# Optimization experiments

Hardware: AMD Instinct MI355X
Metric: run time of the kernel (lower is better)

The kernel has to match this reference:

```python
import jax, jax.numpy as jnp
import numpy as np

N = 16384      # nodes
IN_DIM = 256   # input feature dim
H = 256        # hidden dim
K = 16         # kNN neighbors
L = 2          # GCN layers
C = 10         # classes


def setup_inputs() -> dict:
    key = jax.random.key(0)
    ks = jax.random.split(key, 9)
    s = 0.05
    return {
        "x": jax.random.normal(ks[0], (1, N, IN_DIM), jnp.float32),
        "W_pre": jax.random.normal(ks[1], (H, IN_DIM), jnp.float32) * s,
        "b_pre": jnp.zeros((H,), jnp.float32),
        "W_conv": jax.random.normal(ks[2], (L, H, H), jnp.float32) * s,
        "b_conv": jnp.zeros((L, H), jnp.float32),
        "W_fc1": jax.random.normal(ks[3], (H // 2, H), jnp.float32) * s,
        "b_fc1": jnp.zeros((H // 2,), jnp.float32),
        "W_fc2": jax.random.normal(ks[4], (C, H // 2), jnp.float32) * s,
        "b_fc2": jnp.zeros((C,), jnp.float32),
    }


def _knn_edges(h):
    # h: [N, H]. torch.cdist + topk(k+1, largest=False); squared dist preserves order.
    sq = jnp.sum(h * h, axis=-1)                      # [N]
    d2 = sq[:, None] + sq[None, :] - 2.0 * (h @ h.T)  # [N, N]
    _, idx = jax.lax.top_k(-d2, K + 1)                # smallest k+1
    idx = idx[:, 1:]                                  # drop self, [N, K]
    src = jnp.repeat(jnp.arange(N), K)
    dst = idx.reshape(-1)
    # bidirectional edges (cat with flipped), as in build_knn_graph
    s_idx = jnp.concatenate([src, dst])
    t_idx = jnp.concatenate([dst, src])
    return s_idx, t_idx


def _gcn_layer(h, W, b, s_idx, t_idx, norm):
    m = h @ W.T                                             # PyG GCNConv: lin then propagate
    out = jax.ops.segment_sum(m[s_idx] * norm[:, None], t_idx, num_segments=N)
    return out + b


def reference(x, W_pre, b_pre, W_conv, b_conv, W_fc1, b_fc1, W_fc2, b_fc2):
    # pre_fc (dropout inactive in eval)
    h = jax.nn.relu(x @ W_pre.T + b_pre)   # [1, N, H]
    h0 = h[0]                              # B=1
    s_idx, t_idx = _knn_edges(h0)
    # add self loops (GCNConv default)
    loop = jnp.arange(N)
    s_idx = jnp.concatenate([s_idx, loop])
    t_idx = jnp.concatenate([t_idx, loop])
    # symmetric normalization D^{-1/2} (A+I) D^{-1/2}
    deg = jax.ops.segment_sum(jnp.ones_like(s_idx, dtype=h0.dtype), t_idx, num_segments=N)
    dinv = jnp.where(deg > 0, jax.lax.rsqrt(deg), 0.0)
    norm = dinv[s_idx] * dinv[t_idx]
    hf = h0
    for l in range(L):
        hf = jax.nn.relu(_gcn_layer(hf, W_conv[l], b_conv[l], s_idx, t_idx, norm))
    hf = hf[None]                          # [1, N, H]
    hid = jax.nn.relu(hf @ W_fc1.T + b_fc1)
    pred = hid @ W_fc2.T + b_fc2           # [1, N, C]
    return pred
```

## Files before the change

### kernel.cpp

```cpp
#include <hip/hip_runtime.h>

#define NN   16384
#define DIM  256
#define KNN  16
#define SEG  8
#define JT_PER (NN / SEG / 128)

typedef __attribute__((ext_vector_type(8))) short  bf16x8;
typedef __attribute__((ext_vector_type(4))) float  f32x4;

__device__ __forceinline__ void gload_lds16b(const unsigned short* g, void* l)
{
    __builtin_amdgcn_global_load_lds(
        (const __attribute__((address_space(1))) unsigned int*)g,
        (__attribute__((address_space(3))) unsigned int*)l, 16, 0, 0);
}

__device__ __forceinline__ unsigned short f2bf(float x)
{
    unsigned int u = __float_as_uint(x);
    unsigned int r = (u + 0x7fffu + ((u >> 16) & 1u)) >> 16;
    return (unsigned short)r;
}
__device__ __forceinline__ float bf2f(unsigned short u)
{
    return __uint_as_float(((unsigned)u) << 16);
}

__device__ __forceinline__ unsigned pack_key(float d, int j)
{
    return (__float_as_uint(fmaxf(d, 0.0f)) & 0xFFFFC000u) | (unsigned)j;
}

__global__ __launch_bounds__(256)
void convert_bf16_k(const float* __restrict__ in, unsigned short* __restrict__ out)
{
    const int i4 = blockIdx.x * 256 + threadIdx.x;
    float4 v = *(const float4*)&in[(size_t)i4 * 4];
    ushort4 b;
    b.x = f2bf(v.x); b.y = f2bf(v.y); b.z = f2bf(v.z); b.w = f2bf(v.w);
    *(ushort4*)&out[(size_t)i4 * 4] = b;
}

__global__ __launch_bounds__(256)
void convert_hilo_k(const float* __restrict__ in,
                    unsigned short* __restrict__ hi, unsigned short* __restrict__ lo)
{
    const int i4 = blockIdx.x * 256 + threadIdx.x;
    float4 v = *(const float4*)&in[(size_t)i4 * 4];
    ushort4 h, l;
    h.x = f2bf(v.x); l.x = f2bf(v.x - bf2f(h.x));
    h.y = f2bf(v.y); l.y = f2bf(v.y - bf2f(h.y));
    h.z = f2bf(v.z); l.z = f2bf(v.z - bf2f(h.z));
    h.w = f2bf(v.w); l.w = f2bf(v.w - bf2f(h.w));
    *(ushort4*)&hi[(size_t)i4 * 4] = h;
    *(ushort4*)&lo[(size_t)i4 * 4] = l;
}

__global__ __launch_bounds__(256, 1)
void pre_mfma(const unsigned short* __restrict__ xh, const unsigned short* __restrict__ xl,
              const unsigned short* __restrict__ wh, const unsigned short* __restrict__ wl,
              const float* __restrict__ bias,
              float* __restrict__ C, unsigned short* __restrict__ Cb)
{
    __shared__ __align__(16) float smem[16896];
    unsigned short* stAh = (unsigned short*)smem;
    unsigned short* stAl = (unsigned short*)((char*)smem + 16384);
    unsigned short* stBh = (unsigned short*)((char*)smem + 32768);
    unsigned short* stBl = (unsigned short*)((char*)smem + 49152);
    float* D = smem;

    const int tid  = threadIdx.x;
    const int lane = tid & 63;
    const int wave = tid >> 6;
    const int wj = wave >> 1;
    const int wi = wave & 1;
    const int l15 = lane & 15;
    const int g   = lane >> 4;
    const int R0 = blockIdx.y * 128;
    const int C0 = blockIdx.x * 128;

    f32x4 acc[4][4];
    #pragma unroll
    for (int fa = 0; fa < 4; ++fa)
        #pragma unroll
        for (int fb = 0; fb < 4; ++fb)
            acc[fa][fb] = (f32x4){0.f, 0.f, 0.f, 0.f};

    #pragma unroll 1
    for (int ch = 0; ch < 4; ++ch) {
        const int k0g = ch * 64;
        __syncthreads();
        #pragma unroll
        for (int it = 0; it < 4; ++it) {
            const int lin = tid + it * 256;
            const int row = lin >> 3, f = lin & 7;
            const int kq = f ^ (row & 7);
            gload_lds16b(&xh[(size_t)(R0 + row) * 256 + k0g + kq * 8], (char*)stAh + lin * 16);
            gload_lds16b(&xl[(size_t)(R0 + row) * 256 + k0g + kq * 8], (char*)stAl + lin * 16);
            gload_lds16b(&wh[(size_t)(C0 + row) * 256 + k0g + kq * 8], (char*)stBh + lin * 16);
            gload_lds16b(&wl[(size_t)(C0 + row) * 256 + k0g + kq * 8], (char*)stBl + lin * 16);
        }
        __syncthreads();

        #pragma unroll
        for (int k0 = 0; k0 < 64; k0 += 32) {
            const int ub = (k0 >> 3) + g;
            bf16x8 afh[4], afl[4], bfh[4], bfl[4];
            #pragma unroll
            for (int q = 0; q < 4; ++q) {
                const int jr = wj*64 + q*16 + l15;
                const int ir = wi*64 + q*16 + l15;
                const int oj = (ub ^ (jr & 7)) * 16;
                const int oi = (ub ^ (ir & 7)) * 16;
                afh[q] = *(const bf16x8*)((char*)stBh + jr*128 + oj);
                afl[q] = *(const bf16x8*)((char*)stBl + jr*128 + oj);
                bfh[q] = *(const bf16x8*)((char*)stAh + ir*128 + oi);
                bfl[q] = *(const bf16x8*)((char*)stAl + ir*128 + oi);
            }
            #pragma unroll
            for (int fa = 0; fa < 4; ++fa)
                #pragma unroll
                for (int fb = 0; fb < 4; ++fb) {
                    acc[fa][fb] = __builtin_amdgcn_mfma_f32_16x16x32_bf16(
                        afh[fa], bfl[fb], acc[fa][fb], 0, 0, 0);
                    acc[fa][fb] = __builtin_amdgcn_mfma_f32_16x16x32_bf16(
                        afl[fa], bfh[fb], acc[fa][fb], 0, 0, 0);
                    acc[fa][fb] = __builtin_amdgcn_mfma_f32_16x16x32_bf16(
                        afh[fa], bfh[fb], acc[fa][fb], 0, 0, 0);
                }
        }
    }

    __syncthreads();
    #pragma unroll
    for (int fa = 0; fa < 4; ++fa)
        #pragma unroll
        for (int fb = 0; fb < 4; ++fb) {
            const int i_ = wi*64 + fb*16 + l15;
            const int j0 = wj*64 + fa*16 + g*4;
            *(f32x4*)&D[i_ * 132 + j0] = acc[fa][fb];
        }
    __syncthreads();

    #pragma unroll
    for (int it = 0; it < 16; ++it) {
        const int linear = it * 256 + tid;
        const int r = linear >> 5, c4 = linear & 31;
        float4 v = *(const float4*)&D[r * 132 + c4 * 4];
        float o[4] = {v.x, v.y, v.z, v.w};
        #pragma unroll
        for (int cc = 0; cc < 4; ++cc) {
            o[cc] += bias[C0 + c4*4 + cc];
            o[cc] = fmaxf(o[cc], 0.0f);
        }
        *(float4*)&C[(size_t)(R0 + r) * 256 + C0 + c4*4] =
            make_float4(o[0], o[1], o[2], o[3]);
        ushort4 bv;
        bv.x = f2bf(o[0]); bv.y = f2bf(o[1]);
        bv.z = f2bf(o[2]); bv.w = f2bf(o[3]);
        *(ushort4*)&Cb[(size_t)(R0 + r) * 256 + C0 + c4*4] = bv;
    }
}

template<bool RELU, bool BIAS, bool ROWSCALE, bool F32OUT>
__global__ __launch_bounds__(256, 1)
void gemm_mfma(const unsigned short* __restrict__ Ab, const unsigned short* __restrict__ Wb,
               const float* __restrict__ bias, const float* __restrict__ rscale,
               float* __restrict__ C, unsigned short* __restrict__ Cb, int NO)
{
    __shared__ __align__(16) float smem[25088];
    unsigned short* stA = (unsigned short*)smem;
    unsigned short* stB = (unsigned short*)(smem + 4096);
    float* D = smem + 8192;

    const int tid  = threadIdx.x;
    const int lane = tid & 63;
    const int wave = tid >> 6;
    const int wj = wave >> 1;
    const int wi = wave & 1;
    const int l15 = lane & 15;
    const int g   = lane >> 4;
    const int R0 = blockIdx.y * 128;
    const int C0 = blockIdx.x * 128;

    f32x4 acc[4][4];
    #pragma unroll
    for (int fa = 0; fa < 4; ++fa)
        #pragma unroll
        for (int fb = 0; fb < 4; ++fb)
            acc[fa][fb] = (f32x4){0.f, 0.f, 0.f, 0.f};

    #pragma unroll 1
    for (int ch = 0; ch < 4; ++ch) {
        const int k0g = ch * 64;
        __syncthreads();
        #pragma unroll
        for (int it = 0; it < 4; ++it) {
            const int lin = tid + it * 256;
            const int row = lin >> 3, f = lin & 7;
            const int kq = f ^ (row & 7);
            gload_lds16b(&Ab[(size_t)(R0 + row) * 256 + k0g + kq * 8],
                         (char*)stA + lin * 16);
            gload_lds16b(&Wb[(size_t)(C0 + row) * 256 + k0g + kq * 8],
                         (char*)stB + lin * 16);
        }
        __syncthreads();

        #pragma unroll
        for (int k0 = 0; k0 < 64; k0 += 32) {
            const int ub = (k0 >> 3) + g;
            bf16x8 af[4], bf[4];
            #pragma unroll
            for (int fb = 0; fb < 4; ++fb) {
                const int jr = wj*64 + fb*16 + l15;
                const int ir = wi*64 + fb*16 + l15;
                af[fb] = *(const bf16x8*)((char*)stB + jr*128 + ((ub ^ (jr & 7)) * 16));
                bf[fb] = *(const bf16x8*)((char*)stA + ir*128 + ((ub ^ (ir & 7)) * 16));
            }
            #pragma unroll
            for (int fa = 0; fa < 4; ++fa)
                #pragma unroll
                for (int fb = 0; fb < 4; ++fb)
                    acc[fa][fb] = __builtin_amdgcn_mfma_f32_16x16x32_bf16(
                        af[fa], bf[fb], acc[fa][fb], 0, 0, 0);
        }
    }

    #pragma unroll
    for (int fa = 0; fa < 4; ++fa)
        #pragma unroll
        for (int fb = 0; fb < 4; ++fb) {
            const int i_ = wi*64 + fb*16 + l15;
            const int j0 = wj*64 + fa*16 + g*4;
            *(f32x4*)&D[i_ * 132 + j0] = acc[fa][fb];
        }
    __syncthreads();

    #pragma unroll
    for (int it = 0; it < 16; ++it) {
        const int linear = it * 256 + tid;
        const int r = linear >> 5, c4 = linear & 31;
        float4 v = *(const float4*)&D[r * 132 + c4 * 4];
        const float s = ROWSCALE ? rscale[R0 + r] : 1.0f;
        float o[4] = {v.x * s, v.y * s, v.z * s, v.w * s};
        #pragma unroll
        for (int cc = 0; cc < 4; ++cc) {
            if (BIAS) o[cc] += bias[C0 + c4*4 + cc];
            if (RELU) o[cc] = fmaxf(o[cc], 0.0f);
        }
        if (F32OUT) {
            *(float4*)&C[(size_t)(R0 + r) * NO + C0 + c4*4] =
                make_float4(o[0], o[1], o[2], o[3]);
        } else {
            ushort4 bv;
            bv.x = f2bf(o[0]); bv.y = f2bf(o[1]);
            bv.z = f2bf(o[2]); bv.w = f2bf(o[3]);
            *(ushort4*)&Cb[(size_t)(R0 + r) * NO + C0 + c4*4] = bv;
        }
    }
}

__global__ __launch_bounds__(256)
void sq_kernel(const float* __restrict__ h0, float* __restrict__ sq)
{
    const int wid = threadIdx.x >> 6, lane = threadIdx.x & 63;
    const int row = blockIdx.x * 4 + wid;
    float4 v = *(const float4*)&h0[(size_t)row * DIM + lane * 4];
    float s = v.x*v.x + v.y*v.y + v.z*v.z + v.w*v.w;
    #pragma unroll
    for (int o = 32; o > 0; o >>= 1) s += __shfl_down(s, o);
    if (lane == 0) sq[row] = s;
}

__device__ __forceinline__ void key_insert(unsigned (&kl)[16], unsigned k)
{
    #pragma unroll
    for (int p = 0; p < 16; ++p) {
        const unsigned lo = min(kl[p], k);
        k = max(kl[p], k);
        kl[p] = lo;
    }
}

__global__ __launch_bounds__(256, 3)
void knn_topk(const unsigned short* __restrict__ h0b, const float* __restrict__ sq,
              unsigned* __restrict__ cand)
{
    __shared__ __align__(16) float smem[8704];
    char* sbase = (char*)smem;
    unsigned short* stA = (unsigned short*)sbase;
    unsigned short* stB = (unsigned short*)(sbase + 16384);
    float* D = smem;

    const int tid  = threadIdx.x;
    const int lane = tid & 63;
    const int wave = tid >> 6;
    const int wj = wave >> 1;
    const int wi = wave & 1;
    const int l15 = lane & 15;
    const int g   = lane >> 4;
    const int R0 = blockIdx.y * 128;
    const int seg = blockIdx.x;

    const int orow  = tid >> 1;
    const int ohalf = tid & 1;
    const int myrow = R0 + orow;
    const float osq = sq[myrow];

    unsigned kl[16];
    #pragma unroll
    for (int e = 0; e < 16; ++e) kl[e] = 0xFFFFFFFFu;

    for (int jt = 0; jt < JT_PER; ++jt) {
        const int C0 = seg * (NN / SEG) + jt * 128;
        const bool diag = (C0 == R0);
        f32x4 acc[4][4];
        #pragma unroll
        for (int fa = 0; fa < 4; ++fa)
            #pragma unroll
            for (int fb = 0; fb < 4; ++fb)
                acc[fa][fb] = (f32x4){0.f, 0.f, 0.f, 0.f};

        #pragma unroll 1
        for (int ch = 0; ch < 4; ++ch) {
            const int k0g = ch * 64;
            __syncthreads();
            #pragma unroll
            for (int it = 0; it < 4; ++it) {
                const int lin = tid + it * 256;
                const int row = lin >> 3, f = lin & 7;
                const int kq = f ^ (row & 7);
                gload_lds16b(&h0b[(size_t)(R0 + row) * DIM + k0g + kq * 8],
                             (char*)stA + lin * 16);
                gload_lds16b(&h0b[(size_t)(C0 + row) * DIM + k0g + kq * 8],
                             (char*)stB + lin * 16);
            }
            __syncthreads();

            #pragma unroll
            for (int k0 = 0; k0 < 64; k0 += 32) {
                const int ub = (k0 >> 3) + g;
                bf16x8 af[4], bf[4];
                #pragma unroll
                for (int fb = 0; fb < 4; ++fb) {
                    const int jr = wj*64 + fb*16 + l15;
                    const int ir = wi*64 + fb*16 + l15;
                    af[fb] = *(const bf16x8*)((char*)stB + jr*128 + ((ub ^ (jr & 7)) * 16));
                    bf[fb] = *(const bf16x8*)((char*)stA + ir*128 + ((ub ^ (ir & 7)) * 16));
                }
                #pragma unroll
                for (int fa = 0; fa < 4; ++fa)
                    #pragma unroll
                    for (int fb = 0; fb < 4; ++fb)
                        acc[fa][fb] = __builtin_amdgcn_mfma_f32_16x16x32_bf16(
                            af[fa], bf[fb], acc[fa][fb], 0, 0, 0);
            }
        }

        #pragma unroll 1
        for (int h = 0; h < 2; ++h) {
            __syncthreads();
            if (wj == h) {
                #pragma unroll
                for (int fa = 0; fa < 4; ++fa)
                    #pragma unroll
                    for (int fb = 0; fb < 4; ++fb) {
                        const int i_ = wi*64 + fb*16 + l15;
                        *(f32x4*)&D[i_ * 68 + fa*16 + g*4] = acc[fa][fb];
                    }
            }
            __syncthreads();

            const int cb = C0 + h*64 + ohalf*32;
            const float* Dr = &D[orow * 68 + ohalf * 32];
            #pragma clang loop unroll(disable)
            for (int e = 0; e < 8; ++e) {
                const float4 dv4 = *(const float4*)&Dr[e * 4];
                const float4 sv4 = *(const float4*)&sq[cb + e * 4];
                const int j0 = cb + e * 4;
                unsigned k0 = pack_key((osq + sv4.x) - 2.0f * dv4.x, j0 + 0);
                unsigned k1 = pack_key((osq + sv4.y) - 2.0f * dv4.y, j0 + 1);
                unsigned k2 = pack_key((osq + sv4.z) - 2.0f * dv4.z, j0 + 2);
                unsigned k3 = pack_key((osq + sv4.w) - 2.0f * dv4.w, j0 + 3);
                if (diag) {
                    if (j0 + 0 == myrow) k0 = 0xFFFFFFFFu;
                    if (j0 + 1 == myrow) k1 = 0xFFFFFFFFu;
                    if (j0 + 2 == myrow) k2 = 0xFFFFFFFFu;
                    if (j0 + 3 == myrow) k3 = 0xFFFFFFFFu;
                }
                const unsigned kmin = min(min(k0, k1), min(k2, k3));
                if (kmin < kl[15]) {
                    if (k0 < kl[15]) key_insert(kl, k0);
                    if (k1 < kl[15]) key_insert(kl, k1);
                    if (k2 < kl[15]) key_insert(kl, k2);
                    if (k3 < kl[15]) key_insert(kl, k3);
                }
            }
        }
    }

    __syncthreads();
    unsigned* ck = (unsigned*)smem;
    #pragma unroll
    for (int e = 0; e < 16; ++e) ck[tid * 17 + e] = kl[e];
    __syncthreads();
    if (tid < 128) {
        const unsigned* LA = &ck[(2*tid) * 17];
        const unsigned* LB = &ck[(2*tid + 1) * 17];
        int pa = 0, pb = 0;
        const size_t obase = ((size_t)seg * NN + R0 + tid) * 16;
        #pragma clang loop unroll(disable)
        for (int r = 0; r < 16; ++r) {
            const unsigned ka = LA[pa], kb = LB[pb];
            const bool takeA = (ka < kb);
            cand[obase + r] = takeA ? ka : kb;
            if (takeA) ++pa; else ++pb;
        }
    }
}

__global__ __launch_bounds__(256)
void merge32_k(const unsigned* __restrict__ cand, int* __restrict__ cand32)
{
    const int tid = threadIdx.x;
    const int row = blockIdx.x * 32 + (tid >> 3);
    const int l = tid & 7;
    int head = 0;
    for (int r = 0; r < 32; ++r) {
        const size_t base = ((size_t)l * NN + row) * 16;
        unsigned mk = (head < 16) ? cand[base + head] : 0xFFFFFFFFu;
        int ml = l;
        #pragma unroll
        for (int off = 1; off < 8; off <<= 1) {
            const unsigned ok = __shfl_xor(mk, off);
            const int      ol = __shfl_xor(ml, off);
            if (ok < mk) { mk = ok; ml = ol; }
        }
        if (ml == l) ++head;
        if (l == 0) cand32[(size_t)row * 32 + r] = (int)(mk & 0x3FFFu);
    }
}

__global__ __launch_bounds__(256)
void refine_k(const float* __restrict__ h0, const float* __restrict__ sq,
              const int* __restrict__ cand32, int* __restrict__ nbr)
{
    const int tid = threadIdx.x;
    const int sub = tid & 31;
    const int row = blockIdx.x * 8 + (tid >> 5);
    const int j = cand32[(size_t)row * 32 + sub];
    float dot = 0.0f;
    #pragma clang loop unroll_count(4)
    for (int k = 0; k < DIM; k += 4) {
        float4 a = *(const float4*)&h0[(size_t)row * DIM + k];
        float4 b = *(const float4*)&h0[(size_t)j * DIM + k];
        dot += a.x*b.x + a.y*b.y + a.z*b.z + a.w*b.w;
    }
    float d = sq[row] + sq[j] - 2.0f * dot;
    const int ji = j;
    for (int t = 0; t < 16; ++t) {
        float md = d; int mi = ji;
        #pragma unroll
        for (int off = 1; off < 32; off <<= 1) {
            const float od = __shfl_xor(md, off);
            const int   oi = __shfl_xor(mi, off);
            if (od < md || (od == md && oi < mi)) { md = od; mi = oi; }
        }
        if (d == md && ji == mi) d = 3e38f;
        if (sub == 0) nbr[(size_t)row * KNN + t] = mi;
    }
}

__global__ void count_k(const int* __restrict__ nbr, int* __restrict__ indeg)
{
    const int e = blockIdx.x * 256 + threadIdx.x;
    atomicAdd(&indeg[nbr[e]], 1);
}

__global__ __launch_bounds__(1024)
void scan_k(const int* __restrict__ indeg, int* __restrict__ offs,
            float* __restrict__ dinv)
{
    __shared__ int part[1024];
    const int t = threadIdx.x;
    int pre[16]; int s = 0;
    #pragma unroll
    for (int j = 0; j < 16; ++j) { pre[j] = s; s += indeg[t*16 + j]; }
    part[t] = s;
    __syncthreads();
    for (int d = 1; d < 1024; d <<= 1) {
        int v = (t >= d) ? part[t - d] : 0;
        __syncthreads();
        part[t] += v;
        __syncthreads();
    }
    const int base = (t > 0) ? part[t-1] : 0;
    #pragma unroll
    for (int j = 0; j < 16; ++j) {
        offs[t*16 + j] = base + pre[j];
        dinv[t*16 + j] = rsqrtf((float)(indeg[t*16 + j] + KNN + 1));
    }
}

__global__ void fill_k(const int* __restrict__ nbr, const int* __restrict__ offs,
                       int* __restrict__ cursor, int* __restrict__ rev)
{
    const int e = blockIdx.x * 256 + threadIdx.x;
    const int v = nbr[e];
    const int i = e >> 4;
    const int p = atomicAdd(&cursor[v], 1);
    rev[offs[v] + p] = i;
}

__device__ __forceinline__ void acc_row8(float (&acc)[8], const unsigned short* p)
{
    const uint4 u = *(const uint4*)p;
    acc[0] += __uint_as_float(u.x << 16);
    acc[1] += __uint_as_float(u.x & 0xffff0000u);
    acc[2] += __uint_as_float(u.y << 16);
    acc[3] += __uint_as_float(u.y & 0xffff0000u);
    acc[4] += __uint_as_float(u.z << 16);
    acc[5] += __uint_as_float(u.z & 0xffff0000u);
    acc[6] += __uint_as_float(u.w << 16);
    acc[7] += __uint_as_float(u.w & 0xffff0000u);
}

__global__ __launch_bounds__(256)
void gatherv_k(const unsigned short* __restrict__ mb, const int* __restrict__ nbr,
               const int* __restrict__ rev, const int* __restrict__ offs,
               const int* __restrict__ indeg, const float* __restrict__ dinv,
               const float* __restrict__ bias, unsigned short* __restrict__ outb)
{
    __shared__ float red[8][256];
    const int v   = blockIdx.x;
    const int tid = threadIdx.x;
    const int grp = tid >> 5;
    const int sub = tid & 31;
    const int f0  = sub * 8;

    float acc[8] = {};
    #pragma clang loop unroll(disable)
    for (int t = grp; t < 17; t += 8) {
        const int u = (t == 16) ? v : nbr[(size_t)v * KNN + t];
        acc_row8(acc, &mb[(size_t)u * DIM + f0]);
    }
    const int o = offs[v], n = indeg[v];
    #pragma clang loop unroll_count(2)
    for (int t = grp; t < n; t += 8) {
        acc_row8(acc, &mb[(size_t)rev[o + t] * DIM + f0]);
    }

    #pragma unroll
    for (int e = 0; e < 8; ++e) red[grp][f0 + e] = acc[e];
    __syncthreads();

    float s = 0.0f;
    #pragma unroll
    for (int g2 = 0; g2 < 8; ++g2) s += red[g2][tid];
    const float r = dinv[v] * s + bias[tid];
    outb[(size_t)v * DIM + tid] = f2bf(fmaxf(r, 0.0f));
}

__global__ __launch_bounds__(256)
void fc2_k(const float* __restrict__ hid, const float* __restrict__ W,
           const float* __restrict__ b, float* __restrict__ out)
{
    __shared__ float Ws[1280];
    __shared__ float bs[16];
    const int tid = threadIdx.x;
    for (int i = tid; i < 1280; i += 256) Ws[i] = W[i];
    if (tid < 10) bs[tid] = b[tid];
    __syncthreads();
    const int row = blockIdx.x * 8 + (tid >> 5);
    const int sub = tid & 31;
    float4 h4 = *(const float4*)&hid[(size_t)row * 128 + sub * 4];
    float a[10];
    #pragma unroll
    for (int c = 0; c < 10; ++c) {
        float4 w4 = *(const float4*)&Ws[c * 128 + sub * 4];
        a[c] = h4.x*w4.x + h4.y*w4.y + h4.z*w4.z + h4.w*w4.w;
    }
    #pragma unroll
    for (int off = 16; off >= 1; off >>= 1)
        #pragma unroll
        for (int c = 0; c < 10; ++c) a[c] += __shfl_down(a[c], off, 32);
    if (sub == 0) {
        #pragma unroll
        for (int c = 0; c < 10; ++c) out[(size_t)row * 10 + c] = a[c] + bs[c];
    }
}

extern "C" void kernel_launch(void* const* d_in, const int* in_sizes, int n_in,
                              void* d_out, int out_size, void* d_ws, size_t ws_size,
                              hipStream_t stream)
{
    const float* x     = (const float*)d_in[0];
    const float* Wpre  = (const float*)d_in[1];
    const float* bpre  = (const float*)d_in[2];
    const float* Wconv = (const float*)d_in[3];
    const float* bconv = (const float*)d_in[4];
    const float* Wfc1  = (const float*)d_in[5];
    const float* bfc1  = (const float*)d_in[6];
    const float* Wfc2  = (const float*)d_in[7];
    const float* bfc2  = (const float*)d_in[8];
    float* out = (float*)d_out;

    float* ws    = (float*)d_ws;
    float* h0    = ws;
    float* mbuf  = h0    + (size_t)NN*DIM;
    float* hfbuf = mbuf  + (size_t)NN*DIM;
    float* hid   = hfbuf + (size_t)NN*DIM;
    float* sqv   = hid   + (size_t)NN*128;
    float* dinv  = sqv   + NN;
    int*   nbr   = (int*)(dinv + NN);
    int*   indeg = nbr   + (size_t)NN*KNN;
    int*   offs  = indeg + NN;
    int*   cursor= offs  + NN;
    int*   rev   = cursor+ NN;
    unsigned short* wbc  = (unsigned short*)(rev + (size_t)NN*KNN);
    unsigned short* wbf1 = wbc + 2*256*256;
    unsigned short* wph  = wbf1 + 128*256;
    unsigned short* wpl  = wph + 256*256;

    unsigned short* h0b   = (unsigned short*)hid;
    unsigned short* xh    = (unsigned short*)mbuf;
    unsigned short* xl    = xh + (size_t)NN*DIM;
    unsigned* cand  = (unsigned*)hfbuf;
    int*   cand32 = (int*)mbuf;
    unsigned short* m1b   = (unsigned short*)mbuf;
    unsigned short* m2b   = (unsigned short*)h0;
    unsigned short* hf_b  = (unsigned short*)hfbuf;
    unsigned short* hf2_b = (unsigned short*)(hfbuf + (size_t)NN*DIM/2);

    hipMemsetAsync(indeg,  0, NN*sizeof(int), stream);
    hipMemsetAsync(cursor, 0, NN*sizeof(int), stream);

    convert_hilo_k<<<NN*DIM/1024, 256, 0, stream>>>(x, xh, xl);
    convert_hilo_k<<<DIM*DIM/1024, 256, 0, stream>>>(Wpre, wph, wpl);
    convert_bf16_k<<<2*256*256/1024, 256, 0, stream>>>(Wconv, wbc);
    convert_bf16_k<<<128*256/1024,   256, 0, stream>>>(Wfc1, wbf1);

    pre_mfma<<<dim3(DIM/128, NN/128), 256, 0, stream>>>(
        xh, xl, wph, wpl, bpre, h0, h0b);
    sq_kernel<<<NN/4, 256, 0, stream>>>(h0, sqv);
    knn_topk<<<dim3(SEG, NN/128), 256, 0, stream>>>(h0b, sqv, cand);
    merge32_k<<<NN/32, 256, 0, stream>>>(cand, cand32);
    refine_k<<<NN/8, 256, 0, stream>>>(h0, sqv, cand32, nbr);
    count_k<<<NN*KNN/256, 256, 0, stream>>>(nbr, indeg);
    scan_k<<<1, 1024, 0, stream>>>(indeg, offs, dinv);
    fill_k<<<NN*KNN/256, 256, 0, stream>>>(nbr, offs, cursor, rev);
    gemm_mfma<false,false,true,false><<<dim3(DIM/128, NN/128), 256, 0, stream>>>(
        h0b, wbc, nullptr, dinv, nullptr, m1b, DIM);
    gatherv_k<<<NN, 256, 0, stream>>>(m1b, nbr, rev, offs, indeg, dinv, bconv, hf_b);
    gemm_mfma<false,false,true,false><<<dim3(DIM/128, NN/128), 256, 0, stream>>>(
        hf_b, wbc + 256*256, nullptr, dinv, nullptr, m2b, DIM);
    gatherv_k<<<NN, 256, 0, stream>>>(m2b, nbr, rev, offs, indeg, dinv, bconv + DIM, hf2_b);
    gemm_mfma<true,true,false,true><<<dim3(128/128, NN/128), 256, 0, stream>>>(
        hf2_b, wbf1, bfc1, nullptr, hid, nullptr, 128);
    fc2_k<<<NN/8, 256, 0, stream>>>(hid, Wfc2, bfc2, out);
}
```

Baseline: 819.6 us.

## Fuse kNN merge, refine and degree count; shrink top-k LDS staging

Merges the merge32, refine and count kernels into a single select kernel. Each 32-lane group now does the 8-way candidate merge itself, then computes exact distances and atomically bumps in-degree, so the cand32 and nbr round-trips and two launches go away. Separately, knn_topk now drains the accumulator tile to LDS in four quarter passes instead of two halves, which cuts shared memory per block and may allow more blocks per CU. The cost is extra syncthreads in knn_topk, and the merge is now repeated redundantly across 4 lane groups per row.

```diff
diff --git a/kernel.cpp b/kernel.cpp
--- a/kernel.cpp
+++ b/kernel.cpp
@@ -287,7 +287,7 @@
 void knn_topk(const unsigned short* __restrict__ h0b, const float* __restrict__ sq,
               unsigned* __restrict__ cand)
 {
-    __shared__ __align__(16) float smem[8704];
+    __shared__ __align__(16) float smem[8192];
     char* sbase = (char*)smem;
     unsigned short* stA = (unsigned short*)sbase;
     unsigned short* stB = (unsigned short*)(sbase + 16384);
@@ -359,23 +359,24 @@
         }
 
         #pragma unroll 1
-        for (int h = 0; h < 2; ++h) {
+        for (int p = 0; p < 4; ++p) {
             __syncthreads();
-            if (wj == h) {
+            if (wj == (p >> 1)) {
+                const int fab = 2 * (p & 1);
                 #pragma unroll
-                for (int fa = 0; fa < 4; ++fa)
+                for (int fl = 0; fl < 2; ++fl)
                     #pragma unroll
                     for (int fb = 0; fb < 4; ++fb) {
                         const int i_ = wi*64 + fb*16 + l15;
-                        *(f32x4*)&D[i_ * 68 + fa*16 + g*4] = acc[fa][fb];
+                        *(f32x4*)&D[i_ * 36 + fl*16 + g*4] = acc[fab + fl][fb];
                     }
             }
             __syncthreads();
 
-            const int cb = C0 + h*64 + ohalf*32;
-            const float* Dr = &D[orow * 68 + ohalf * 32];
+            const int cb = C0 + p*32 + ohalf*16;
+            const float* Dr = &D[orow * 36 + ohalf * 16];
             #pragma clang loop unroll(disable)
-            for (int e = 0; e < 8; ++e) {
+            for (int e = 0; e < 4; ++e) {
                 const float4 dv4 = *(const float4*)&Dr[e * 4];
                 const float4 sv4 = *(const float4*)&sq[cb + e * 4];
                 const int j0 = cb + e * 4;
@@ -421,35 +422,35 @@
 }
 
 __global__ __launch_bounds__(256)
-void merge32_k(const unsigned* __restrict__ cand, int* __restrict__ cand32)
-{
-    const int tid = threadIdx.x;
-    const int row = blockIdx.x * 32 + (tid >> 3);
-    const int l = tid & 7;
-    int head = 0;
-    for (int r = 0; r < 32; ++r) {
-        const size_t base = ((size_t)l * NN + row) * 16;
-        unsigned mk = (head < 16) ? cand[base + head] : 0xFFFFFFFFu;
-        int ml = l;
-        #pragma unroll
-        for (int off = 1; off < 8; off <<= 1) {
-            const unsigned ok = __shfl_xor(mk, off);
-            const int      ol = __shfl_xor(ml, off);
-            if (ok < mk) { mk = ok; ml = ol; }
-        }
-        if (ml == l) ++head;
-        if (l == 0) cand32[(size_t)row * 32 + r] = (int)(mk & 0x3FFFu);
-    }
-}
-
-__global__ __launch_bounds__(256)
-void refine_k(const float* __restrict__ h0, const float* __restrict__ sq,
-              const int* __restrict__ cand32, int* __restrict__ nbr)
+void select_k(const unsigned* __restrict__ cand, const float* __restrict__ h0,
+              const float* __restrict__ sq, int* __restrict__ nbr,
+              int* __restrict__ indeg)
 {
     const int tid = threadIdx.x;
     const int sub = tid & 31;
     const int row = blockIdx.x * 8 + (tid >> 5);
-    const int j = cand32[(size_t)row * 32 + sub];
+
+    int myj = 0;
+    {
+        const int l8 = sub & 7;
+        const size_t base = ((size_t)l8 * NN + row) * 16;
+        int head = 0;
+        #pragma clang loop unroll(disable)
+        for (int r = 0; r < 32; ++r) {
+            unsigned mk = (head < 16) ? cand[base + head] : 0xFFFFFFFFu;
+            int ml = l8;
+            #pragma unroll
+            for (int off = 1; off < 8; off <<= 1) {
+                const unsigned ok = __shfl_xor(mk, off);
+                const int      ol = __shfl_xor(ml, off);
+                if (ok < mk) { mk = ok; ml = ol; }
+            }
+            if (r == sub) myj = (int)(mk & 0x3FFFu);
+            if (ml == l8) ++head;
+        }
+    }
+
+    const int j = myj;
     float dot = 0.0f;
     #pragma clang loop unroll_count(4)
     for (int k = 0; k < DIM; k += 4) {
@@ -458,6 +459,7 @@
         dot += a.x*b.x + a.y*b.y + a.z*b.z + a.w*b.w;
     }
     float d = sq[row] + sq[j] - 2.0f * dot;
+
     const int ji = j;
     for (int t = 0; t < 16; ++t) {
         float md = d; int mi = ji;
@@ -468,14 +470,11 @@
             if (od < md || (od == md && oi < mi)) { md = od; mi = oi; }
         }
         if (d == md && ji == mi) d = 3e38f;
-        if (sub == 0) nbr[(size_t)row * KNN + t] = mi;
-    }
-}
-
-__global__ void count_k(const int* __restrict__ nbr, int* __restrict__ indeg)
-{
-    const int e = blockIdx.x * 256 + threadIdx.x;
-    atomicAdd(&indeg[nbr[e]], 1);
+        if (sub == 0) {
+            nbr[(size_t)row * KNN + t] = mi;
+            atomicAdd(&indeg[mi], 1);
+        }
+    }
 }
 
 __global__ __launch_bounds__(1024)
@@ -627,7 +626,6 @@
     unsigned short* xh    = (unsigned short*)mbuf;
     unsigned short* xl    = xh + (size_t)NN*DIM;
     unsigned* cand  = (unsigned*)hfbuf;
-    int*   cand32 = (int*)mbuf;
     unsigned short* m1b   = (unsigned short*)mbuf;
     unsigned short* m2b   = (unsigned short*)h0;
     unsigned short* hf_b  = (unsigned short*)hfbuf;
@@ -645,9 +643,7 @@
         xh, xl, wph, wpl, bpre, h0, h0b);
     sq_kernel<<<NN/4, 256, 0, stream>>>(h0, sqv);
     knn_topk<<<dim3(SEG, NN/128), 256, 0, stream>>>(h0b, sqv, cand);
-    merge32_k<<<NN/32, 256, 0, stream>>>(cand, cand32);
-    refine_k<<<NN/8, 256, 0, stream>>>(h0, sqv, cand32, nbr);
-    count_k<<<NN*KNN/256, 256, 0, stream>>>(nbr, indeg);
+    select_k<<<NN/8, 256, 0, stream>>>(cand, h0, sqv, nbr, indeg);
     scan_k<<<1, 1024, 0, stream>>>(indeg, offs, dinv);
     fill_k<<<NN*KNN/256, 256, 0, stream>>>(nbr, offs, cursor, rev);
     gemm_mfma<false,false,true,false><<<dim3(DIM/128, NN/128), 256, 0, stream>>>(
```

Measured after the change: 1.420 ms. +73.2%, slower.
